# Performance work log

Hardware: AMD Instinct MI355X
Metric: run time of the kernel (lower is better)

Reference implementation:

```python
import jax, jax.numpy as jnp
import numpy as np

B, OBS, NH, LAT = 8192, 256, 2048, 128

def setup_inputs() -> dict:
    key = jax.random.key(0)
    k1, k2, k3, k4, k5, k6 = jax.random.split(key, 6)
    s1 = 1.0 / np.sqrt(OBS + NH)
    s2 = 1.0 / np.sqrt(NH)
    return {
        "x": jax.random.normal(k1, (B, OBS), dtype=jnp.float32),
        "h": jax.random.normal(k2, (B, NH), dtype=jnp.float32),
        "W_i2h": jax.random.normal(k3, (NH, OBS + NH), dtype=jnp.float32) * s1,
        "b_i2h": jax.random.normal(k4, (NH,), dtype=jnp.float32) * s1,
        "W_h2o": jax.random.normal(k5, (2 * LAT, NH), dtype=jnp.float32) * s2,
        "b_h2o": jax.random.normal(k6, (2 * LAT,), dtype=jnp.float32) * s2,
    }

def reference(x, h, W_i2h, b_i2h, W_h2o, b_h2o):
    # combined = cat((x, h), dim=1)  -> [B, OBS+NH]
    combined = jnp.concatenate([x, h], axis=1)
    # h_new = tanh(i2h(combined));  Linear is y = x @ W.T + b
    h_new = jnp.tanh(combined @ W_i2h.T + b_i2h)
    out = h_new @ W_h2o.T + b_h2o  # [B, 2*LAT]
    return (out, h_new)
```

## Files before the change

### kernel.cpp

```cpp
#include <hip/hip_runtime.h>
#include <hip/hip_bf16.h>
#include <cstdint>

using bf16 = __hip_bfloat16;
typedef __attribute__((ext_vector_type(8))) short short8;
typedef __attribute__((ext_vector_type(4))) float floatx4;

static constexpr int BATCH = 8192;
static constexpr int K1    = 2304;
static constexpr int N1    = 2048;
static constexpr int K2    = 2048;
static constexpr int N2    = 256;
static constexpr int KT1   = K1 / 64;

__device__ __forceinline__ void gload_lds16(const void* g, void* l) {
  __builtin_amdgcn_global_load_lds(
      (const __attribute__((address_space(1))) void*)g,
      (__attribute__((address_space(3))) void*)l, 16, 0, 0);
}

__device__ __forceinline__ float fast_tanh(float x) {
  float e = __builtin_amdgcn_exp2f(x * 2.8853900817779268f);
  return 1.0f - 2.0f * __builtin_amdgcn_rcpf(e + 1.0f);
}

__device__ __forceinline__ short8 cvt8(const float* src) {
  float4 a = ((const float4*)src)[0];
  float4 b = ((const float4*)src)[1];
  union { short8 v; bf16 e[8]; } u;
  u.e[0] = __float2bfloat16(a.x); u.e[1] = __float2bfloat16(a.y);
  u.e[2] = __float2bfloat16(a.z); u.e[3] = __float2bfloat16(a.w);
  u.e[4] = __float2bfloat16(b.x); u.e[5] = __float2bfloat16(b.y);
  u.e[6] = __float2bfloat16(b.z); u.e[7] = __float2bfloat16(b.w);
  return u.v;
}

static constexpr int SEG0 = BATCH * (K1 / 8);
static constexpr int SEG1 = N1 * K1 / 8;
static constexpr int SEG2 = N2 * K2 / 8;
static constexpr int SEG3 = BATCH * (N2 / 4);
__global__ __launch_bounds__(256) void prep(
    const float* __restrict__ x, const float* __restrict__ h,
    const float* __restrict__ W1, const float* __restrict__ W2,
    const float* __restrict__ b2,
    bf16* __restrict__ comb, bf16* __restrict__ W1b, bf16* __restrict__ W2b,
    float* __restrict__ outp) {
  int i = blockIdx.x * 256 + threadIdx.x;
  if (i < SEG0) {
    int row  = i / 288;
    int slot = i - row * 288;
    const float* src = (slot < 32) ? (x + (size_t)row * 256 + slot * 8)
                                   : (h + (size_t)row * 2048 + (slot - 32) * 8);
    *(short8*)(comb + (size_t)row * 2304 + slot * 8) = cvt8(src);
  } else if (i < SEG0 + SEG1) {
    int j = i - SEG0;
    *(short8*)(W1b + (size_t)j * 8) = cvt8(W1 + (size_t)j * 8);
  } else if (i < SEG0 + SEG1 + SEG2) {
    int j = i - (SEG0 + SEG1);
    *(short8*)(W2b + (size_t)j * 8) = cvt8(W2 + (size_t)j * 8);
  } else {
    int j = i - (SEG0 + SEG1 + SEG2);
    float4 b = ((const float4*)b2)[j & 63];
    ((float4*)outp)[j] = b;
  }
}

__global__ __launch_bounds__(512, 2) void gemm1_tanh(
    const bf16* __restrict__ A, const bf16* __restrict__ W,
    const float* __restrict__ bias,
    float* __restrict__ hf32, bf16* __restrict__ hb16) {
  __shared__ bf16 lds[2][2][2][8192];
  const int t    = threadIdx.x;
  const int lane = t & 63;
  const int wave = t >> 6;
  const int wm   = (wave >> 2) * 128;
  const int wn   = (wave & 3) * 64;
  const int quad = lane >> 4;
  const int r15  = lane & 15;

  const int swz   = ((quad ^ ((r15 >> 1) & 3)) << 4);
  const int baseA = wm * 64 + r15 * 64 + swz;
  const int baseB = 32768 + wn * 64 + r15 * 64 + swz;

  const int srow  = t >> 2;
  const int sslot = t & 3;
  const int sq    = (sslot ^ ((srow >> 1) & 3)) * 8;

  const size_t Abase = (size_t)blockIdx.x * 256 * K1;
  const size_t Bbase = (size_t)blockIdx.y * 256 * K1;
  const size_t gA0 = Abase + (size_t)srow * K1 + sq;
  const size_t gA1 = Abase + (size_t)(srow + 128) * K1 + sq;
  const size_t gB0 = Bbase + (size_t)srow * K1 + sq;
  const size_t gB1 = Bbase + (size_t)(srow + 128) * K1 + sq;
  const int d0 = t * 16, d1 = 8192 + t * 16;
  char* const ldsb = (char*)lds;

#define STAGE2(sb, skh, skt) do {                                            \
    const int ktc_ = ((skt) < KT1 ? (skt) : (KT1 - 1));                      \
    const size_t ko_ = (size_t)ktc_ * 64 + (skh) * 32;                       \
    char* const la_ = ldsb + ((sb) << 16) + ((skh) << 14);                   \
    gload_lds16(A + gA0 + ko_, la_ + d0);                                    \
    gload_lds16(A + gA1 + ko_, la_ + d1);                                    \
    gload_lds16(W + gB0 + ko_, la_ + 32768 + d0);                            \
    gload_lds16(W + gB1 + ko_, la_ + 32768 + d1);                            \
  } while (0)

  floatx4 acc[8][4];
  const floatx4 z = {0.f, 0.f, 0.f, 0.f};
#pragma unroll
  for (int i = 0; i < 8; i++)
#pragma unroll
    for (int j = 0; j < 4; j++) acc[i][j] = z;

  STAGE2(0, 0, 0); STAGE2(0, 1, 0); STAGE2(1, 0, 1);
  asm volatile("s_waitcnt vmcnt(4)" ::: "memory");
  __builtin_amdgcn_s_barrier();

#define MPHASE(cb, ks, sb, skh, skt, VMW) do {                               \
    STAGE2(sb, skh, skt);                                                    \
    __builtin_amdgcn_sched_barrier(0);                                       \
    if (VMW) asm volatile("s_waitcnt vmcnt(8)" ::: "memory");                \
    __builtin_amdgcn_s_barrier();                                            \
    asm volatile("" ::: "memory");          \
    const char* Lb_ = ldsb + ((cb) << 16) + ((ks) << 14);                    \
    short8 bf_[4], af0_[4], af1_[4];                                         \
    _Pragma("unroll")                                                        \
    for (int nt = 0; nt < 4; ++nt)                                           \
      bf_[nt] = *(const short8*)(Lb_ + baseB + nt * 1024);                   \
    _Pragma("unroll")                                                        \
    for (int mt = 0; mt < 4; ++mt)                                           \
      af0_[mt] = *(const short8*)(Lb_ + baseA + mt * 1024);                  \
    __builtin_amdgcn_sched_barrier(0);                                       \
    _Pragma("unroll")                                                        \
    for (int mt = 0; mt < 4; ++mt)                                           \
      af1_[mt] = *(const short8*)(Lb_ + baseA + 4096 + mt * 1024);           \
    __builtin_amdgcn_sched_barrier(0);                                       \
    asm volatile("s_waitcnt lgkmcnt(4)" ::: "memory");                       \
    __builtin_amdgcn_sched_barrier(0);                                       \
    __builtin_amdgcn_s_setprio(1);                                           \
    _Pragma("unroll")                                                        \
    for (int mt = 0; mt < 4; ++mt)                                           \
      _Pragma("unroll")                                                      \
      for (int nt = 0; nt < 4; ++nt)                                         \
        acc[mt][nt] = __builtin_amdgcn_mfma_f32_16x16x32_bf16(               \
            af0_[mt], bf_[nt], acc[mt][nt], 0, 0, 0);                        \
    __builtin_amdgcn_s_setprio(0);                                           \
    asm volatile("s_waitcnt lgkmcnt(0)" ::: "memory");                       \
    __builtin_amdgcn_sched_barrier(0);                                       \
    __builtin_amdgcn_s_setprio(1);                                           \
    _Pragma("unroll")                                                        \
    for (int mt = 0; mt < 4; ++mt)                                           \
      _Pragma("unroll")                                                      \
      for (int nt = 0; nt < 4; ++nt)                                         \
        acc[4 + mt][nt] = __builtin_amdgcn_mfma_f32_16x16x32_bf16(           \
            af1_[mt], bf_[nt], acc[4 + mt][nt], 0, 0, 0);                    \
    __builtin_amdgcn_s_setprio(0);                                           \
    __builtin_amdgcn_s_barrier();                                            \
  } while (0)

#pragma clang loop unroll(disable)
  for (int t2 = 0; t2 < KT1 / 2; ++t2) {
    const int n = 2 * t2;
    MPHASE(0, 0,  1, 1, n + 1, 0);
    MPHASE(0, 1,  0, 0, n + 2, 1);
    MPHASE(1, 0,  0, 1, n + 2, 0);
    MPHASE(1, 1,  1, 0, n + 3, 1);
  }
#undef MPHASE
#undef STAGE2

  const int gcol0 = blockIdx.y * 256 + wn;
  float bv[4];
#pragma unroll
  for (int nt = 0; nt < 4; ++nt) bv[nt] = bias[gcol0 + nt * 16 + r15];
  const size_t grow0 = (size_t)blockIdx.x * 256 + wm;
#pragma unroll
  for (int mt = 0; mt < 8; ++mt) {
#pragma unroll
    for (int i = 0; i < 4; ++i) {
      const size_t gr = grow0 + mt * 16 + quad * 4 + i;
      const size_t rb = gr * (size_t)N1;
#pragma unroll
      for (int nt = 0; nt < 4; ++nt) {
        const int gc = gcol0 + nt * 16 + r15;
        float v = fast_tanh(acc[mt][nt][i] + bv[nt]);
        hf32[rb + gc] = v;
        hb16[rb + gc] = __float2bfloat16(v);
      }
    }
  }
}

__global__ __launch_bounds__(256) void gemm2_out(
    const bf16* __restrict__ A, const bf16* __restrict__ W,
    float* __restrict__ out) {
  __shared__ bf16 As[2][32 * 64];
  __shared__ bf16 Bs[2][256 * 64];
  const int t    = threadIdx.x;
  const int lane = t & 63;
  const int wave = t >> 6;
  const int quad = lane >> 4;
  const int r15  = lane & 15;
  const int srow = t >> 3;
  const int sc   = t & 7;

  const int mrow0 = blockIdx.x * 32;
  const int kbase = blockIdx.y * (K2 / 2);

#define G2STAGE(b, kt) do {                                                  \
    const int k0_ = kbase + (kt) * 64;                                       \
    {                                                                        \
      int gc_ = k0_ + ((sc ^ (srow & 7)) << 3);                              \
      gload_lds16(A + (size_t)(mrow0 + srow) * K2 + gc_,                     \
                  (char*)As[b] + t * 16);                                    \
    }                                                                        \
    _Pragma("unroll")                                                        \
    for (int it = 0; it < 8; ++it) {                                         \
      int row_ = it * 32 + srow;                                             \
      int gc_  = k0_ + ((sc ^ (row_ & 7)) << 3);                             \
      gload_lds16(W + (size_t)row_ * K2 + gc_,                               \
                  (char*)Bs[b] + it * 4096 + t * 16);                        \
    }                                                                        \
  } while (0)

  floatx4 acc[2][4];
  const floatx4 z = {0.f, 0.f, 0.f, 0.f};
#pragma unroll
  for (int i = 0; i < 2; i++)
#pragma unroll
    for (int j = 0; j < 4; j++) acc[i][j] = z;

  G2STAGE(0, 0);
#pragma clang loop unroll(disable)
  for (int kt = 0; kt < 16; ++kt) {
    const int cur = kt & 1;
    if (kt + 1 < 16) {
      G2STAGE(cur ^ 1, kt + 1);
      asm volatile("s_waitcnt vmcnt(9)" ::: "memory");
    } else {
      asm volatile("s_waitcnt vmcnt(0)" ::: "memory");
    }
    __builtin_amdgcn_s_barrier();
    asm volatile("" ::: "memory");
#pragma unroll
    for (int ks = 0; ks < 2; ++ks) {
      short8 af[2], bfr[4];
      const int kq = ks * 4 + quad;
#pragma unroll
      for (int mt = 0; mt < 2; ++mt) {
        int row = mt * 16 + r15;
        af[mt] = *(const short8*)((const char*)As[cur] + row * 128 +
                                  ((kq ^ (row & 7)) << 4));
      }
#pragma unroll
      for (int nt = 0; nt < 4; ++nt) {
        int row = wave * 64 + nt * 16 + r15;
        bfr[nt] = *(const short8*)((const char*)Bs[cur] + row * 128 +
                                   ((kq ^ (row & 7)) << 4));
      }
#pragma unroll
      for (int mt = 0; mt < 2; ++mt)
#pragma unroll
        for (int nt = 0; nt < 4; ++nt)
          acc[mt][nt] = __builtin_amdgcn_mfma_f32_16x16x32_bf16(
              af[mt], bfr[nt], acc[mt][nt], 0, 0, 0);
    }
    asm volatile("" ::: "memory");
    __builtin_amdgcn_s_barrier();
  }
#undef G2STAGE

  const int gcol0 = wave * 64;
#pragma unroll
  for (int mt = 0; mt < 2; ++mt) {
#pragma unroll
    for (int i = 0; i < 4; ++i) {
      size_t gr = (size_t)mrow0 + mt * 16 + quad * 4 + i;
      size_t rb = gr * (size_t)N2;
#pragma unroll
      for (int nt = 0; nt < 4; ++nt) {
        int gc = gcol0 + nt * 16 + r15;
        unsafeAtomicAdd(&out[rb + gc], acc[mt][nt][i]);
      }
    }
  }
}

extern "C" void kernel_launch(void* const* d_in, const int* in_sizes, int n_in,
                              void* d_out, int out_size, void* d_ws,
                              size_t ws_size, hipStream_t stream) {
  const float* x     = (const float*)d_in[0];
  const float* h     = (const float*)d_in[1];
  const float* W_i2h = (const float*)d_in[2];
  const float* b_i2h = (const float*)d_in[3];
  const float* W_h2o = (const float*)d_in[4];
  const float* b_h2o = (const float*)d_in[5];

  float* out       = (float*)d_out;
  float* hnew_f32  = out + (size_t)BATCH * N2;

  bf16* comb   = (bf16*)d_ws;
  bf16* Wi2h_b = comb + (size_t)BATCH * K1;
  bf16* Wh2o_b = Wi2h_b + (size_t)N1 * K1;
  bf16* hnew_b = Wh2o_b + (size_t)N2 * K2;

  prep<<<(SEG0 + SEG1 + SEG2 + SEG3) / 256, 256, 0, stream>>>(
      x, h, W_i2h, W_h2o, b_h2o, comb, Wi2h_b, Wh2o_b, out);

  gemm1_tanh<<<dim3(BATCH / 256, N1 / 256), 512, 0, stream>>>(
      comb, Wi2h_b, b_i2h, hnew_f32, hnew_b);

  gemm2_out<<<dim3(BATCH / 32, 2), 256, 0, stream>>>(hnew_b, Wh2o_b, out);
}
```

Before: 260.2 us.

## Software-pipeline LDS fragment reads one phase ahead with double-buffered registers

Restructures the GEMM1 main loop into eight half-phases. Each half-phase issues the LDS fragment loads for the next half-phase into alternate register sets (afA/afB, bfA/bfB) while it runs MFMAs on the current ones. Global-to-LDS staging is split per matrix (A or W) and spread across more phases, with adjusted vmcnt/lgkmcnt waits. The aim is to hide LDS read latency behind MFMA work and to smooth out global load issue. In exchange it uses more registers and adds a barrier per half-phase, and the tighter waitcnt logic risks races if the counts are wrong.

```diff
diff --git a/kernel.cpp b/kernel.cpp
--- a/kernel.cpp
+++ b/kernel.cpp
@@ -95,14 +95,14 @@
   const int d0 = t * 16, d1 = 8192 + t * 16;
   char* const ldsb = (char*)lds;
 
-#define STAGE2(sb, skh, skt) do {                                            \
+#define STG(sb, mat_, skh, skt) do {                                         \
     const int ktc_ = ((skt) < KT1 ? (skt) : (KT1 - 1));                      \
     const size_t ko_ = (size_t)ktc_ * 64 + (skh) * 32;                       \
-    char* const la_ = ldsb + ((sb) << 16) + ((skh) << 14);                   \
-    gload_lds16(A + gA0 + ko_, la_ + d0);                                    \
-    gload_lds16(A + gA1 + ko_, la_ + d1);                                    \
-    gload_lds16(W + gB0 + ko_, la_ + 32768 + d0);                            \
-    gload_lds16(W + gB1 + ko_, la_ + 32768 + d1);                            \
+    char* const la_ = ldsb + ((sb) << 16) + ((mat_) * 32768) + ((skh) << 14);\
+    const bf16* g0_ = (mat_) ? (W + gB0 + ko_) : (A + gA0 + ko_);            \
+    const bf16* g1_ = (mat_) ? (W + gB1 + ko_) : (A + gA1 + ko_);            \
+    gload_lds16(g0_, la_ + d0);                                              \
+    gload_lds16(g1_, la_ + d1);                                              \
   } while (0)
 
   floatx4 acc[8][4];
@@ -112,62 +112,65 @@
 #pragma unroll
     for (int j = 0; j < 4; j++) acc[i][j] = z;
 
-  STAGE2(0, 0, 0); STAGE2(0, 1, 0); STAGE2(1, 0, 1);
-  asm volatile("s_waitcnt vmcnt(4)" ::: "memory");
+  short8 afA[4], afB[4], bfA[4], bfB[4];
+
+  STG(0, 0, 0, 0); STG(0, 1, 0, 0);
+  STG(0, 0, 1, 0); STG(0, 1, 1, 0);
+  STG(1, 0, 0, 1); STG(1, 1, 0, 1);
+  asm volatile("s_waitcnt vmcnt(8)" ::: "memory");
   __builtin_amdgcn_s_barrier();
-
-#define MPHASE(cb, ks, sb, skh, skt, VMW) do {                               \
-    STAGE2(sb, skh, skt);                                                    \
-    __builtin_amdgcn_sched_barrier(0);                                       \
-    if (VMW) asm volatile("s_waitcnt vmcnt(8)" ::: "memory");                \
-    __builtin_amdgcn_s_barrier();                                            \
-    asm volatile("" ::: "memory");          \
-    const char* Lb_ = ldsb + ((cb) << 16) + ((ks) << 14);                    \
-    short8 bf_[4], af0_[4], af1_[4];                                         \
-    _Pragma("unroll")                                                        \
-    for (int nt = 0; nt < 4; ++nt)                                           \
-      bf_[nt] = *(const short8*)(Lb_ + baseB + nt * 1024);                   \
+  __builtin_amdgcn_sched_barrier(0);
+  {
+#pragma unroll
+    for (int mt = 0; mt < 4; ++mt)
+      afA[mt] = *(const short8*)(ldsb + baseA + mt * 1024);
+#pragma unroll
+    for (int nt = 0; nt < 4; ++nt)
+      bfA[nt] = *(const short8*)(ldsb + baseB + nt * 1024);
+  }
+
+#define PH(ccb, cks, cmtg, AFC, BFC, rcb, rks, rmtg, AFN, BFN, RB,           \
+           sb, smat, skh, skt, VMW, LGS) do {                                \
+    const char* Lr_ = ldsb + ((rcb) << 16) + ((rks) << 14);                  \
     _Pragma("unroll")                                                        \
     for (int mt = 0; mt < 4; ++mt)                                           \
-      af0_[mt] = *(const short8*)(Lb_ + baseA + mt * 1024);                  \
+      AFN[mt] = *(const short8*)(Lr_ + baseA + (rmtg) * 4096 + mt * 1024);   \
+    if (RB) {                                                                \
+      _Pragma("unroll")                                                      \
+      for (int nt = 0; nt < 4; ++nt)                                         \
+        BFN[nt] = *(const short8*)(Lr_ + baseB + nt * 1024);                 \
+    }                                                                        \
+    STG(sb, smat, skh, skt);                                                 \
     __builtin_amdgcn_sched_barrier(0);                                       \
-    _Pragma("unroll")                                                        \
-    for (int mt = 0; mt < 4; ++mt)                                           \
-      af1_[mt] = *(const short8*)(Lb_ + baseA + 4096 + mt * 1024);           \
-    __builtin_amdgcn_sched_barrier(0);                                       \
-    asm volatile("s_waitcnt lgkmcnt(4)" ::: "memory");                       \
+    if (VMW) asm volatile("s_waitcnt vmcnt(6)" ::: "memory");                \
+    asm volatile("s_waitcnt lgkmcnt(" LGS ")" ::: "memory");                 \
     __builtin_amdgcn_sched_barrier(0);                                       \
     __builtin_amdgcn_s_setprio(1);                                           \
     _Pragma("unroll")                                                        \
     for (int mt = 0; mt < 4; ++mt)                                           \
       _Pragma("unroll")                                                      \
       for (int nt = 0; nt < 4; ++nt)                                         \
-        acc[mt][nt] = __builtin_amdgcn_mfma_f32_16x16x32_bf16(               \
-            af0_[mt], bf_[nt], acc[mt][nt], 0, 0, 0);                        \
-    __builtin_amdgcn_s_setprio(0);                                           \
-    asm volatile("s_waitcnt lgkmcnt(0)" ::: "memory");                       \
-    __builtin_amdgcn_sched_barrier(0);                                       \
-    __builtin_amdgcn_s_setprio(1);                                           \
-    _Pragma("unroll")                                                        \
-    for (int mt = 0; mt < 4; ++mt)                                           \
-      _Pragma("unroll")                                                      \
-      for (int nt = 0; nt < 4; ++nt)                                         \
-        acc[4 + mt][nt] = __builtin_amdgcn_mfma_f32_16x16x32_bf16(           \
-            af1_[mt], bf_[nt], acc[4 + mt][nt], 0, 0, 0);                    \
+        acc[(cmtg) * 4 + mt][nt] = __builtin_amdgcn_mfma_f32_16x16x32_bf16(  \
+            AFC[mt], BFC[nt], acc[(cmtg) * 4 + mt][nt], 0, 0, 0);            \
     __builtin_amdgcn_s_setprio(0);                                           \
     __builtin_amdgcn_s_barrier();                                            \
+    __builtin_amdgcn_sched_barrier(0);                                       \
   } while (0)
 
 #pragma clang loop unroll(disable)
   for (int t2 = 0; t2 < KT1 / 2; ++t2) {
     const int n = 2 * t2;
-    MPHASE(0, 0,  1, 1, n + 1, 0);
-    MPHASE(0, 1,  0, 0, n + 2, 1);
-    MPHASE(1, 0,  0, 1, n + 2, 0);
-    MPHASE(1, 1,  1, 0, n + 3, 1);
-  }
-#undef MPHASE
-#undef STAGE2
+    PH(0, 0, 0, afA, bfA,  0, 0, 1, afB, bfB, 0,  1, 0, 1, n + 1, 1, "4");
+    PH(0, 0, 1, afB, bfA,  0, 1, 0, afA, bfB, 1,  1, 1, 1, n + 1, 0, "8");
+    PH(0, 1, 0, afA, bfB,  0, 1, 1, afB, bfA, 0,  0, 0, 0, n + 2, 1, "4");
+    PH(0, 1, 1, afB, bfB,  1, 0, 0, afA, bfA, 1,  0, 1, 0, n + 2, 0, "8");
+    PH(1, 0, 0, afA, bfA,  1, 0, 1, afB, bfB, 0,  0, 0, 1, n + 2, 1, "4");
+    PH(1, 0, 1, afB, bfA,  1, 1, 0, afA, bfB, 1,  0, 1, 1, n + 2, 0, "8");
+    PH(1, 1, 0, afA, bfB,  1, 1, 1, afB, bfA, 0,  1, 0, 0, n + 3, 1, "4");
+    PH(1, 1, 1, afB, bfB,  0, 0, 0, afA, bfA, 1,  1, 1, 0, n + 3, 0, "8");
+  }
+#undef PH
+#undef STG
 
   const int gcol0 = blockIdx.y * 256 + wn;
   float bv[4];
```

Result: no change. 256.1 us (-1.6%).
